# Kernel optimization log

Measured on AMD Instinct MI355X. Metric: run time of the kernel, lower is better.

Reference implementation:

```python
import jax, jax.numpy as jnp
import numpy as np

NEG = -9e15

def setup_inputs() -> dict:
    key = jax.random.key(0)
    k1, k2, k3, k4, k5 = jax.random.split(key, 5)
    N, Fin, Fout = 8192, 256, 128
    h = jax.random.normal(k1, (N, Fin), dtype=jnp.float32)
    adj = jax.random.randint(k2, (N, N), 0, 2, dtype=jnp.int32)
    # Parameters (xavier_uniform with gain=1.414 for a1/a2; kaiming-like for W is fine as random init)
    lim_w = float(np.sqrt(6.0 / (Fin + Fout)))
    W = jax.random.uniform(k3, (Fout, Fin), dtype=jnp.float32, minval=-lim_w, maxval=lim_w)
    lim_a = float(1.414 * np.sqrt(6.0 / (Fout + 1)))
    a1 = jax.random.uniform(k4, (Fout, 1), dtype=jnp.float32, minval=-lim_a, maxval=lim_a)
    a2 = jax.random.uniform(k5, (Fout, 1), dtype=jnp.float32, minval=-lim_a, maxval=lim_a)
    return {"h": h, "adj": adj, "W": W, "a1": a1, "a2": a2}

def reference(h, adj, W, a1, a2):
    Wh = h @ W.T                                   # [N, Fout]
    s1 = (Wh @ a1)                                 # [N, 1]
    s2 = (Wh @ a2)                                 # [N, 1]
    e = jax.nn.leaky_relu(s1 + s2.T, 0.2)          # [N, N]
    att = jnp.where(adj > 0, e, jnp.float32(NEG))
    att = jax.nn.softmax(att, axis=1)
    h_prime = att @ Wh                             # [N, Fout]
    return jax.nn.elu(h_prime)
```

## Files before the change

kernel.cpp:

```cpp
#include <hip/hip_runtime.h>
#include <cstdint>
#include <cstddef>

#define N_NODES 8192
#define FIN 256
#define FOUT 128
#define MT 32
#define KC 256
#define JS 4
#define JW (N_NODES / JS)
#define NCHS (JW / KC)
#define LOG2E 1.4426950408889634f

typedef __attribute__((ext_vector_type(8))) short bf16x8;
typedef __attribute__((ext_vector_type(4))) float f32x4;
typedef __attribute__((ext_vector_type(4))) int i32x4;
typedef __attribute__((ext_vector_type(2))) unsigned int u32x2;
typedef __attribute__((ext_vector_type(4))) unsigned int u32x4;

__device__ __forceinline__ float bf2f(unsigned short u) {
    union { unsigned int i; float f; } v; v.i = ((unsigned int)u) << 16; return v.f;
}
__device__ __forceinline__ unsigned short f2bf(float f) {
    union { float f; unsigned int i; } v; v.f = f;
    unsigned int r = (v.i + 0x7FFFu + ((v.i >> 16) & 1u)) >> 16;
    return (unsigned short)r;
}
__device__ __forceinline__ unsigned int pack_bf16(float a, float b) {
    return (unsigned)f2bf(a) | ((unsigned)f2bf(b) << 16);
}

__device__ __forceinline__ size_t whb_idx(int j, int f) {
    return ((size_t)((j >> 5) * 8 + (f >> 4)) << 9) + (((j >> 3) & 3) << 7)
         + ((f & 15) << 3) + (j & 7);
}

__global__ __launch_bounds__(256) void wh_kernel(const float* __restrict__ h,
                                                 const float* __restrict__ W,
                                                 const float* __restrict__ a1,
                                                 const float* __restrict__ a2,
                                                 unsigned short* __restrict__ whB,
                                                 float* __restrict__ s1p,
                                                 float* __restrict__ s2p) {
    __shared__ __align__(16) unsigned short hB[64][264];
    __shared__ __align__(16) unsigned short wLds[16 * 64 * 8];
    const int t = threadIdx.x;
    const int i0 = blockIdx.x * 64;
    const int f0 = blockIdx.y * 32;
#pragma unroll
    for (int c = 0; c < 8; ++c) {
        int chunk = c * 256 + t;
        int row = chunk >> 5;
        int g8  = chunk & 31;
        const float* hp = &h[(size_t)(i0 + row) * FIN + g8 * 8];
        f32x4 v0 = *(const f32x4*)hp;
        f32x4 v1 = *(const f32x4*)(hp + 4);
        u32x4 pk;
        pk.x = pack_bf16(v0[0], v0[1]); pk.y = pack_bf16(v0[2], v0[3]);
        pk.z = pack_bf16(v1[0], v1[1]); pk.w = pack_bf16(v1[2], v1[3]);
        *(u32x4*)&hB[row][g8 * 8] = pk;
    }
    {
        const int kk = t & 7;
        const int fr = t >> 3;
        const int fh = fr >> 4;
        const float* wr = W + (size_t)(f0 + fr) * FIN + kk * 32;
#pragma unroll
        for (int g = 0; g < 4; ++g) {
            f32x4 v0 = *(const f32x4*)(wr + g * 8);
            f32x4 v1 = *(const f32x4*)(wr + g * 8 + 4);
            u32x4 pk;
            pk.x = pack_bf16(v0[0], v0[1]); pk.y = pack_bf16(v0[2], v0[3]);
            pk.z = pack_bf16(v1[0], v1[1]); pk.w = pack_bf16(v1[2], v1[3]);
            *(u32x4*)&wLds[(size_t)(((kk * 2 + fh) * 64) + (fr & 15) + g * 16) * 8] = pk;
        }
    }
    __syncthreads();
    const int lane = t & 63;
    const int wv = t >> 6;
    const int quad = lane >> 4;
    const int sl = lane & 15;
    f32x4 acc0 = {0.f,0.f,0.f,0.f}, acc1 = {0.f,0.f,0.f,0.f};
#pragma unroll
    for (int kk = 0; kk < 8; ++kk) {
        bf16x8 A  = *(const bf16x8*)&hB[wv * 16 + sl][kk * 32 + quad * 8];
        bf16x8 B0 = *(const bf16x8*)&wLds[(size_t)((kk * 2 + 0) * 64 + lane) * 8];
        bf16x8 B1 = *(const bf16x8*)&wLds[(size_t)((kk * 2 + 1) * 64 + lane) * 8];
        acc0 = __builtin_amdgcn_mfma_f32_16x16x32_bf16(A, B0, acc0, 0, 0, 0);
        acc1 = __builtin_amdgcn_mfma_f32_16x16x32_bf16(A, B1, acc1, 0, 0, 0);
    }
    const float a1v0 = a1[f0 + sl], a1v1 = a1[f0 + 16 + sl];
    const float a2v0 = a2[f0 + sl], a2v1 = a2[f0 + 16 + sl];
    float c1[4], c2[4];
#pragma unroll
    for (int r = 0; r < 4; ++r) {
        int i = i0 + wv * 16 + quad * 4 + r;
        whB[whb_idx(i, f0 + sl)]      = f2bf(acc0[r]);
        whB[whb_idx(i, f0 + 16 + sl)] = f2bf(acc1[r]);
        c1[r] = acc0[r] * a1v0 + acc1[r] * a1v1;
        c2[r] = acc0[r] * a2v0 + acc1[r] * a2v1;
    }
#pragma unroll
    for (int r = 0; r < 4; ++r) {
        c1[r] += __shfl_xor(c1[r], 1); c2[r] += __shfl_xor(c2[r], 1);
        c1[r] += __shfl_xor(c1[r], 2); c2[r] += __shfl_xor(c2[r], 2);
        c1[r] += __shfl_xor(c1[r], 4); c2[r] += __shfl_xor(c2[r], 4);
        c1[r] += __shfl_xor(c1[r], 8); c2[r] += __shfl_xor(c2[r], 8);
    }
    if (sl == 0) {
#pragma unroll
        for (int r = 0; r < 4; ++r) {
            int i = i0 + wv * 16 + quad * 4 + r;
            s1p[(size_t)blockIdx.y * N_NODES + i] = c1[r] * LOG2E;
            s2p[(size_t)blockIdx.y * N_NODES + i] = c2[r] * LOG2E;
        }
    }
}

__global__ __launch_bounds__(256) void gat_kernel(const int* __restrict__ adj,
                                                  const unsigned short* __restrict__ whB,
                                                  const float* __restrict__ s1p,
                                                  const float* __restrict__ s2p,
                                                  float* __restrict__ out,
                                                  float* __restrict__ nums,
                                                  float* __restrict__ dens) {
    __shared__ __align__(16) unsigned short sP[MT][KC + 8];
    __shared__ __align__(16) float sS2[JW];
    __shared__ float sDen[MT];
    __shared__ float sS1[MT];
    const int t = threadIdx.x;
    const int slice = blockIdx.x & (JS - 1);
    const int i0 = (blockIdx.x >> 2) * MT;
    const int jb = slice * JW;
    const int kb0 = slice * (JW / 32);
    float* __restrict__ num = slice ? (nums + (size_t)(slice - 1) * N_NODES * FOUT) : out;
    float* __restrict__ den = dens + (size_t)slice * N_NODES;

    {
        const float* p0 = s2p + jb + t * 8;
        f32x4 a = {0.f, 0.f, 0.f, 0.f}, b = {0.f, 0.f, 0.f, 0.f};
#pragma unroll
        for (int pb = 0; pb < 4; ++pb) {
            a += *(const f32x4*)(p0 + (size_t)pb * N_NODES);
            b += *(const f32x4*)(p0 + (size_t)pb * N_NODES + 4);
        }
        *(f32x4*)&sS2[t * 8]     = a;
        *(f32x4*)&sS2[t * 8 + 4] = b;
    }
    if (t < MT) {
        float a = 0.f;
#pragma unroll
        for (int pb = 0; pb < 4; ++pb) a += s1p[(size_t)pb * N_NODES + i0 + t];
        sS1[t] = a;
        sDen[t] = 0.f;
    }
    __syncthreads();

    const int r0 = t >> 4;
    const int s  = t & 15;
    const int lane = t & 63;
    const int quad = lane >> 4;
    const int sl = lane & 15;
    const int wv = t >> 6;
    const int* __restrict__ aRow0 = adj + (size_t)(i0 + r0) * N_NODES + jb;
    const int* __restrict__ aRow1 = aRow0 + (size_t)16 * N_NODES;
    const float s1a = sS1[r0];
    const float s1b = sS1[r0 + 16];

    f32x4 acc00 = {0.f,0.f,0.f,0.f}, acc01 = {0.f,0.f,0.f,0.f};
    f32x4 acc10 = {0.f,0.f,0.f,0.f}, acc11 = {0.f,0.f,0.f,0.f};

    for (int ch = 0; ch < NCHS; ++ch) {
        const int cb = ch * KC + s * 16;
        i32x4 av0[4], av1[4];
        f32x4 sv[4];
#pragma unroll
        for (int q = 0; q < 4; ++q) {
            av0[q] = *(const i32x4*)&aRow0[cb + q * 4];
            av1[q] = *(const i32x4*)&aRow1[cb + q * 4];
            sv[q]  = *(const f32x4*)&sS2[cb + q * 4];
        }
        float part0 = 0.f, part1 = 0.f;
        unsigned int w0[8], w1[8];
#pragma unroll
        for (int q = 0; q < 4; ++q) {
            float p0[4], p1v[4];
#pragma unroll
            for (int r = 0; r < 4; ++r) {
                float y0 = s1a + sv[q][r];
                float y1 = s1b + sv[q][r];
                y0 = fmaxf(y0, 0.2f * y0);
                y1 = fmaxf(y1, 0.2f * y1);
                float e0 = __builtin_amdgcn_exp2f(y0);
                float e1 = __builtin_amdgcn_exp2f(y1);
                p0[r]  = (av0[q][r] > 0) ? e0 : 0.f;
                p1v[r] = (av1[q][r] > 0) ? e1 : 0.f;
                part0 += p0[r];
                part1 += p1v[r];
            }
            w0[2 * q]     = pack_bf16(p0[0], p0[1]);
            w0[2 * q + 1] = pack_bf16(p0[2], p0[3]);
            w1[2 * q]     = pack_bf16(p1v[0], p1v[1]);
            w1[2 * q + 1] = pack_bf16(p1v[2], p1v[3]);
        }
        u32x4 ra = {w0[0], w0[1], w0[2], w0[3]};
        u32x4 rb = {w0[4], w0[5], w0[6], w0[7]};
        u32x4 rc = {w1[0], w1[1], w1[2], w1[3]};
        u32x4 rd = {w1[4], w1[5], w1[6], w1[7]};
        *(u32x4*)&sP[r0][s * 16]          = ra;
        *(u32x4*)&sP[r0][s * 16 + 8]      = rb;
        *(u32x4*)&sP[r0 + 16][s * 16]     = rc;
        *(u32x4*)&sP[r0 + 16][s * 16 + 8] = rd;
        part0 += __shfl_xor(part0, 1); part1 += __shfl_xor(part1, 1);
        part0 += __shfl_xor(part0, 2); part1 += __shfl_xor(part1, 2);
        part0 += __shfl_xor(part0, 4); part1 += __shfl_xor(part1, 4);
        part0 += __shfl_xor(part0, 8); part1 += __shfl_xor(part1, 8);
        if (s == 0) { sDen[r0] += part0; sDen[r0 + 16] += part1; }
        __syncthreads();
#pragma unroll
        for (int kq = 0; kq < KC / 32; ++kq) {
            bf16x8 a0  = *(const bf16x8*)&sP[sl][kq * 32 + quad * 8];
            bf16x8 a1f = *(const bf16x8*)&sP[16 + sl][kq * 32 + quad * 8];
            int kb = kb0 + ch * (KC / 32) + kq;
            const unsigned short* t0 = whB + ((size_t)(kb * 8 + wv * 2) << 9) + lane * 8;
            bf16x8 b0 = *(const bf16x8*)t0;
            bf16x8 b1 = *(const bf16x8*)(t0 + 512);
            acc00 = __builtin_amdgcn_mfma_f32_16x16x32_bf16(a0,  b0, acc00, 0, 0, 0);
            acc01 = __builtin_amdgcn_mfma_f32_16x16x32_bf16(a0,  b1, acc01, 0, 0, 0);
            acc10 = __builtin_amdgcn_mfma_f32_16x16x32_bf16(a1f, b0, acc10, 0, 0, 0);
            acc11 = __builtin_amdgcn_mfma_f32_16x16x32_bf16(a1f, b1, acc11, 0, 0, 0);
        }
        __syncthreads();
    }
    if (t < MT) den[i0 + t] = sDen[t];
#pragma unroll
    for (int m = 0; m < 2; ++m) {
#pragma unroll
        for (int nn = 0; nn < 2; ++nn) {
            f32x4 a = (m == 0) ? (nn == 0 ? acc00 : acc01) : (nn == 0 ? acc10 : acc11);
#pragma unroll
            for (int r = 0; r < 4; ++r) {
                int row = m * 16 + quad * 4 + r;
                num[(size_t)(i0 + row) * FOUT + wv * 32 + nn * 16 + sl] = a[r];
            }
        }
    }
}

__global__ __launch_bounds__(256) void fin_kernel(float* __restrict__ out,
                                                  const float* __restrict__ nums,
                                                  const float* __restrict__ dens) {
    const int idx4 = blockIdx.x * 256 + threadIdx.x;
    const int idx = idx4 * 4;
    const int i = idx >> 7;
    const size_t NF = (size_t)N_NODES * FOUT;
    f32x4 n0 = *(f32x4*)&out[idx];
    f32x4 n1 = *(const f32x4*)&nums[idx];
    f32x4 n2 = *(const f32x4*)&nums[NF + idx];
    f32x4 n3 = *(const f32x4*)&nums[2 * NF + idx];
    float denv = dens[i] + dens[N_NODES + i] + dens[2 * N_NODES + i] + dens[3 * N_NODES + i];
    float dv = fmaxf(denv, 1e-30f);
    f32x4 r;
#pragma unroll
    for (int k = 0; k < 4; ++k) {
        float numv = (n0[k] + n1[k]) + (n2[k] + n3[k]);
        float v = numv / dv;
        r[k] = (v > 0.f) ? v : expm1f(v);
    }
    *(f32x4*)&out[idx] = r;
}

extern "C" void kernel_launch(void* const* d_in, const int* in_sizes, int n_in,
                              void* d_out, int out_size, void* d_ws, size_t ws_size,
                              hipStream_t stream) {
    const float* h   = (const float*)d_in[0];
    const int*   adj = (const int*)d_in[1];
    const float* W   = (const float*)d_in[2];
    const float* a1  = (const float*)d_in[3];
    const float* a2  = (const float*)d_in[4];

    char* ws = (char*)d_ws;
    unsigned short* whB = (unsigned short*)ws;
    float* s1p  = (float*)(ws + (4u << 20));
    float* s2p  = s1p + 4 * N_NODES;
    float* dens = s2p + 4 * N_NODES;
    float* nums = dens + 4 * N_NODES;
    float* out  = (float*)d_out;

    wh_kernel<<<dim3(N_NODES / 64, FOUT / 32), 256, 0, stream>>>(h, W, a1, a2,
                                                                 whB, s1p, s2p);
    gat_kernel<<<dim3((N_NODES / MT) * JS), 256, 0, stream>>>(adj, whB, s1p, s2p,
                                                              out, nums, dens);
    fin_kernel<<<dim3(N_NODES * FOUT / 1024), 256, 0, stream>>>(out, nums, dens);
}
```

Baseline: 382.6 us.

## Fuse the split-K finalize into the attention kernel with a last-block atomic counter

The separate finalize kernel is removed. Each attention block now writes its partial numerators to workspace and atomically increments a per-row-tile counter. The fourth (last) block for a row tile sums the four partial numerators and denominators, normalizes, applies ELU and writes the output. This drops one kernel launch and the extra full-grid pass, but adds atomics, threadfences and a tail of serialized reduction work per tile, and the final reads use the MFMA fragment layout rather than wide vector loads.

```diff
diff --git a/kernel.cpp b/kernel.cpp
--- a/kernel.cpp
+++ b/kernel.cpp
@@ -41,12 +41,14 @@
                                                  const float* __restrict__ a2,
                                                  unsigned short* __restrict__ whB,
                                                  float* __restrict__ s1p,
-                                                 float* __restrict__ s2p) {
+                                                 float* __restrict__ s2p,
+                                                 int* __restrict__ cnt) {
     __shared__ __align__(16) unsigned short hB[64][264];
     __shared__ __align__(16) unsigned short wLds[16 * 64 * 8];
     const int t = threadIdx.x;
     const int i0 = blockIdx.x * 64;
     const int f0 = blockIdx.y * 32;
+    if (blockIdx.x == 0 && blockIdx.y == 0) cnt[t] = 0;
 #pragma unroll
     for (int c = 0; c < 8; ++c) {
         int chunk = c * 256 + t;
@@ -121,19 +123,22 @@
                                                   const unsigned short* __restrict__ whB,
                                                   const float* __restrict__ s1p,
                                                   const float* __restrict__ s2p,
-                                                  float* __restrict__ out,
                                                   float* __restrict__ nums,
-                                                  float* __restrict__ dens) {
+                                                  float* __restrict__ dens,
+                                                  int* __restrict__ cnt,
+                                                  float* __restrict__ out) {
     __shared__ __align__(16) unsigned short sP[MT][KC + 8];
     __shared__ __align__(16) float sS2[JW];
     __shared__ float sDen[MT];
     __shared__ float sS1[MT];
+    __shared__ int sRank;
     const int t = threadIdx.x;
     const int slice = blockIdx.x & (JS - 1);
     const int i0 = (blockIdx.x >> 2) * MT;
     const int jb = slice * JW;
     const int kb0 = slice * (JW / 32);
-    float* __restrict__ num = slice ? (nums + (size_t)(slice - 1) * N_NODES * FOUT) : out;
+    const size_t NF = (size_t)N_NODES * FOUT;
+    float* __restrict__ num = nums + (size_t)slice * NF;
     float* __restrict__ den = dens + (size_t)slice * N_NODES;
 
     {
@@ -245,29 +250,35 @@
             }
         }
     }
-}
-
-__global__ __launch_bounds__(256) void fin_kernel(float* __restrict__ out,
-                                                  const float* __restrict__ nums,
-                                                  const float* __restrict__ dens) {
-    const int idx4 = blockIdx.x * 256 + threadIdx.x;
-    const int idx = idx4 * 4;
-    const int i = idx >> 7;
-    const size_t NF = (size_t)N_NODES * FOUT;
-    f32x4 n0 = *(f32x4*)&out[idx];
-    f32x4 n1 = *(const f32x4*)&nums[idx];
-    f32x4 n2 = *(const f32x4*)&nums[NF + idx];
-    f32x4 n3 = *(const f32x4*)&nums[2 * NF + idx];
-    float denv = dens[i] + dens[N_NODES + i] + dens[2 * N_NODES + i] + dens[3 * N_NODES + i];
-    float dv = fmaxf(denv, 1e-30f);
-    f32x4 r;
-#pragma unroll
-    for (int k = 0; k < 4; ++k) {
-        float numv = (n0[k] + n1[k]) + (n2[k] + n3[k]);
-        float v = numv / dv;
-        r[k] = (v > 0.f) ? v : expm1f(v);
-    }
-    *(f32x4*)&out[idx] = r;
+    __syncthreads();
+    if (t == 0) {
+        __threadfence();
+        sRank = atomicAdd(&cnt[blockIdx.x >> 2], 1);
+    }
+    __syncthreads();
+    if (sRank != 3) return;
+    __threadfence();
+    if (t < MT) {
+        float d0 = dens[i0 + t],               d1 = dens[N_NODES + i0 + t];
+        float d2 = dens[2 * N_NODES + i0 + t], d3 = dens[3 * N_NODES + i0 + t];
+        sDen[t] = fmaxf(((d0 + d1) + d2) + d3, 1e-30f);
+    }
+    __syncthreads();
+#pragma unroll
+    for (int m = 0; m < 2; ++m) {
+#pragma unroll
+        for (int nn = 0; nn < 2; ++nn) {
+#pragma unroll
+            for (int r = 0; r < 4; ++r) {
+                int row = m * 16 + quad * 4 + r;
+                size_t off = (size_t)(i0 + row) * FOUT + wv * 32 + nn * 16 + sl;
+                float n0 = nums[off],          n1 = nums[NF + off];
+                float n2 = nums[2 * NF + off], n3 = nums[3 * NF + off];
+                float v = ((n0 + n1) + (n2 + n3)) / sDen[row];
+                out[off] = (v > 0.f) ? v : expm1f(v);
+            }
+        }
+    }
 }
 
 extern "C" void kernel_launch(void* const* d_in, const int* in_sizes, int n_in,
@@ -281,6 +292,7 @@
 
     char* ws = (char*)d_ws;
     unsigned short* whB = (unsigned short*)ws;
+    int* cnt    = (int*)(ws + (3u << 20));
     float* s1p  = (float*)(ws + (4u << 20));
     float* s2p  = s1p + 4 * N_NODES;
     float* dens = s2p + 4 * N_NODES;
@@ -288,8 +300,7 @@
     float* out  = (float*)d_out;
 
     wh_kernel<<<dim3(N_NODES / 64, FOUT / 32), 256, 0, stream>>>(h, W, a1, a2,
-                                                                 whB, s1p, s2p);
+                                                                 whB, s1p, s2p, cnt);
     gat_kernel<<<dim3((N_NODES / MT) * JS), 256, 0, stream>>>(adj, whB, s1p, s2p,
-                                                              out, nums, dens);
-    fin_kernel<<<dim3(N_NODES * FOUT / 1024), 256, 0, stream>>>(out, nums, dens);
-}
+                                                              nums, dens, cnt, out);
+}
```

Result: slower. 485.4 us (+26.9%).
